# Performance work log

Hardware: AMD Instinct MI355X
Metric: run time of the kernel (lower is better)

Reference implementation:

```python
import jax, jax.numpy as jnp
import numpy as np

D_MODEL = 512
N_HEADS = 8
D_FF = 2048
B, L = 4, 2048
EPS = 1e-5


def _layernorm(x, g, b):
    mu = jnp.mean(x, axis=-1, keepdims=True)
    var = jnp.mean(jnp.square(x - mu), axis=-1, keepdims=True)
    return (x - mu) * jax.lax.rsqrt(var + EPS) * g + b


def setup_inputs() -> dict:
    key = jax.random.key(0)
    ks = jax.random.split(key, 8)
    s = 0.02
    return {
        'x': jax.random.normal(ks[0], (B, L, D_MODEL), jnp.float32),
        'Wq': jax.random.normal(ks[1], (D_MODEL, D_MODEL), jnp.float32) * s,
        'bq': jnp.zeros((D_MODEL,), jnp.float32),
        'Wk': jax.random.normal(ks[2], (D_MODEL, D_MODEL), jnp.float32) * s,
        'bk': jnp.zeros((D_MODEL,), jnp.float32),
        'Wv': jax.random.normal(ks[3], (D_MODEL, D_MODEL), jnp.float32) * s,
        'bv': jnp.zeros((D_MODEL,), jnp.float32),
        'Wo': jax.random.normal(ks[4], (D_MODEL, D_MODEL), jnp.float32) * s,
        'bo': jnp.zeros((D_MODEL,), jnp.float32),
        'W1': jax.random.normal(ks[5], (D_MODEL, D_FF), jnp.float32) * s,
        'b1': jnp.zeros((D_FF,), jnp.float32),
        'W2': jax.random.normal(ks[6], (D_FF, D_MODEL), jnp.float32) * s,
        'b2': jnp.zeros((D_MODEL,), jnp.float32),
        'g1': jnp.ones((D_MODEL,), jnp.float32),
        'be1': jnp.zeros((D_MODEL,), jnp.float32),
        'g2': jnp.ones((D_MODEL,), jnp.float32),
        'be2': jnp.zeros((D_MODEL,), jnp.float32),
    }


def reference(x, Wq, bq, Wk, bk, Wv, bv, Wo, bo, W1, b1, W2, b2, g1, be1, g2, be2):
    B_, L_, D = x.shape
    H = N_HEADS
    E = D // H
    q = (x @ Wq + bq).reshape(B_, L_, H, E)
    k = (x @ Wk + bk).reshape(B_, L_, H, E)
    v = (x @ Wv + bv).reshape(B_, L_, H, E)
    scale = 1.0 / jnp.sqrt(jnp.float32(E))
    # full [B,H,L,S] scores (mask_flag=False -> no causal mask)
    scores = jnp.einsum('blhe,bshe->bhls', q, k)
    A = jax.nn.softmax(scale * scores, axis=-1)
    V = jnp.einsum('bhls,bshd->blhd', A, v).reshape(B_, L_, D)
    attn_out = V @ Wo + bo
    x = _layernorm(x + attn_out, g1, be1)
    h = jax.nn.gelu(x @ W1 + b1, approximate=False)  # torch nn.GELU default = exact erf
    x = _layernorm(x + (h @ W2 + b2), g2, be2)
    return x
```

## Files before the change

kernel.cpp:

```cpp
#include <hip/hip_runtime.h>
#include <math.h>

#define DM 512
#define LSEQ 2048
#define BATCH 4
#define NH 8
#define EH 64
#define DFF 2048
#define MTOK (BATCH*LSEQ)
#define QKVW 1536
#define QSCL 0.18033688011112042f

using short8  = __attribute__((ext_vector_type(8))) short;
using floatx4 = __attribute__((ext_vector_type(4))) float;

__device__ __forceinline__ short f2b(float f) {
    unsigned u = __float_as_uint(f);
    return (short)((u + 0x7FFFu + ((u >> 16) & 1u)) >> 16);
}
__device__ __forceinline__ float b2f(short s) {
    return __uint_as_float(((unsigned)(unsigned short)s) << 16);
}
__device__ __forceinline__ unsigned pack2bf(float lo, float hi) {
    return __builtin_amdgcn_perm(__float_as_uint(hi) + 0x8000u,
                                 __float_as_uint(lo) + 0x8000u, 0x07060302u);
}
__device__ __forceinline__ float gelu_tanh(float v) {
    float v2 = v * v;
    float y  = v * fmaf(0.0356774081f, v2, 0.7978845608f);
    float e  = __builtin_amdgcn_exp2f(y * 2.885390082f);
    float r  = __builtin_amdgcn_rcpf(e + 1.0f);
    return v * (1.0f - r);
}
__device__ __forceinline__ void load_lds16(const short* g, short* l) {
    __builtin_amdgcn_global_load_lds(
        (const __attribute__((address_space(1))) void*)g,
        (__attribute__((address_space(3))) void*)l, 16, 0, 0);
}
#define MFMA_BF16(a, b, c) __builtin_amdgcn_mfma_f32_16x16x32_bf16(a, b, c, 0, 0, 0)

__global__ __launch_bounds__(256) void prep_kernel(
    const float* __restrict__ Wq, const float* __restrict__ Wk,
    const float* __restrict__ Wv, const float* __restrict__ Wo,
    const float* __restrict__ W1, const float* __restrict__ W2,
    const float* __restrict__ x,
    const float* __restrict__ bq, const float* __restrict__ bk,
    const float* __restrict__ bv,
    short* __restrict__ Wqkvt, short* __restrict__ Wot,
    short* __restrict__ W1t, short* __restrict__ W2t,
    short* __restrict__ xb, float* __restrict__ bqkv)
{
    __shared__ float t[64][65];
    const int bid = blockIdx.x;
    const int tid = threadIdx.x;

    if (bid >= 2880) {
        #pragma unroll
        for (int j = 0; j < 6; ++j) {
            const int i = j * 256 + tid;
            bqkv[i] = (i < 512) ? bq[i] : (i < 1024 ? bk[i - 512] : bv[i - 1024]);
        }
        return;
    }
    if (bid >= 832) {
        const long i = ((long)(bid - 832) * 256 + tid) * 8;
        float4 a = *(const float4*)(x + i);
        float4 b = *(const float4*)(x + i + 4);
        short tt[8] = { f2b(a.x), f2b(a.y), f2b(a.z), f2b(a.w),
                        f2b(b.x), f2b(b.y), f2b(b.z), f2b(b.w) };
        *(float4*)(xb + i) = *(float4*)tt;
        return;
    }
    const float* src; short* dst; int C, R, bx, by;
    if (bid < 256) {
        const int w = bid >> 6, sub = bid & 63;
        src = (w == 0) ? Wq : (w == 1) ? Wk : Wv;
        dst = Wqkvt + (long)w * 262144;
        R = 512; C = 512; bx = sub & 7; by = sub >> 3;
    } else if (bid < 320) {
        const int sub = bid - 256;
        src = Wo; dst = Wot; R = 512; C = 512; bx = sub & 7; by = sub >> 3;
    } else if (bid < 576) {
        const int sub = bid - 320;
        src = W1; dst = W1t; R = 512; C = 2048; bx = sub & 31; by = sub >> 5;
    } else {
        const int sub = bid - 576;
        src = W2; dst = W2t; R = 2048; C = 512; bx = sub & 7; by = sub >> 3;
    }
    const int r0 = by * 64, c0 = bx * 64;
    const int r = tid >> 2, cs = (tid & 3) * 16;
    const float* ip = src + (long)(r0 + r) * C + c0 + cs;
    #pragma unroll
    for (int i = 0; i < 4; ++i) {
        float4 v = *(const float4*)(ip + i * 4);
        t[r][cs + i*4 + 0] = v.x; t[r][cs + i*4 + 1] = v.y;
        t[r][cs + i*4 + 2] = v.z; t[r][cs + i*4 + 3] = v.w;
    }
    __syncthreads();
    short tmp[16];
    #pragma unroll
    for (int j = 0; j < 16; ++j) tmp[j] = f2b(t[cs + j][r]);
    short* op = dst + (long)(c0 + r) * R + r0 + cs;
    *(float4*)op       = *(float4*)&tmp[0];
    *(float4*)(op + 8) = *(float4*)&tmp[8];
}

template<int TN, int DO_GELU, int QKV>
__global__ __launch_bounds__(256, 4) void mfma_gemm(
    const short* __restrict__ A, const short* __restrict__ Bt,
    const float* __restrict__ bias, short* __restrict__ C,
    short* __restrict__ VtOut, int M, int N, int K, int lda, int ldc)
{
    constexpr int NJ = TN / 32;
    constexpr int NB = TN / 64;
    __shared__ short As[2][128][32];
    __shared__ short Bs[2][TN][32];

    const int tid  = threadIdx.x;
    const int wave = tid >> 6;
    const int lane = tid & 63;
    const int qd   = lane >> 4;
    const int sl   = lane & 15;
    const int m0 = blockIdx.y * 128;
    const int n0 = blockIdx.x * TN;
    const int wm = (wave & 1) * 64;
    const int wn = (wave >> 1) * (TN / 2);
    const int srow = lane >> 2;
    const int scol = (lane & 3) * 8;

    floatx4 acc[4][NJ];
    const floatx4 fz = {0.f, 0.f, 0.f, 0.f};
    #pragma unroll
    for (int i = 0; i < 4; ++i)
        #pragma unroll
        for (int j = 0; j < NJ; ++j) acc[i][j] = fz;

    const short* Abase = A  + (long)m0 * lda + scol;
    const short* Bbase = Bt + (long)n0 * K   + scol;

    #pragma unroll
    for (int it = 0; it < 2; ++it) {
        const int rg = wave * 2 + it;
        load_lds16(Abase + (long)(rg*16 + srow) * lda, &As[0][rg * 16][0]);
    }
    #pragma unroll
    for (int it = 0; it < NB; ++it) {
        const int rg = wave * NB + it;
        load_lds16(Bbase + (long)(rg*16 + srow) * K, &Bs[0][rg * 16][0]);
    }

    const int NIT = K / 32;
    for (int kit = 0; kit < NIT; ++kit) {
        const int cur = kit & 1;
        __syncthreads();
        if (kit + 1 < NIT) {
            const int nk = (kit + 1) * 32;
            #pragma unroll
            for (int it = 0; it < 2; ++it) {
                const int rg = wave * 2 + it;
                load_lds16(Abase + (long)(rg*16 + srow) * lda + nk, &As[1 - cur][rg * 16][0]);
            }
            #pragma unroll
            for (int it = 0; it < NB; ++it) {
                const int rg = wave * NB + it;
                load_lds16(Bbase + (long)(rg*16 + srow) * K + nk, &Bs[1 - cur][rg * 16][0]);
            }
        }
        short8 af[4], bf[NJ];
        #pragma unroll
        for (int t = 0; t < 4; ++t)
            af[t] = *(const short8*)&As[cur][wm + t*16 + sl][qd * 8];
        #pragma unroll
        for (int t = 0; t < NJ; ++t)
            bf[t] = *(const short8*)&Bs[cur][wn + t*16 + sl][qd * 8];
        #pragma unroll
        for (int i = 0; i < 4; ++i)
            #pragma unroll
            for (int j = 0; j < NJ; ++j)
                acc[i][j] = MFMA_BF16(af[i], bf[j], acc[i][j]);
    }

    #pragma unroll
    for (int j = 0; j < NJ; ++j) {
        const int col = n0 + wn + j*16 + sl;
        const float bvs = bias[col];
        #pragma unroll
        for (int i = 0; i < 4; ++i) {
            float v[4];
            #pragma unroll
            for (int r = 0; r < 4; ++r) {
                float tv = acc[i][j][r] + bvs;
                if (DO_GELU) tv = gelu_tanh(tv);
                v[r] = tv;
            }
            const int row0 = m0 + wm + i*16 + qd*4;
            if (QKV) {
                if (col < 1024) {
                    const float s = (col < 512) ? QSCL : 1.0f;
                    #pragma unroll
                    for (int r = 0; r < 4; ++r)
                        C[(long)(row0 + r) * 1024 + col] = f2b(v[r] * s);
                } else {
                    const int e = col - 1024;
                    const int b_ = row0 >> 11, l0 = row0 & 2047;
                    uint2 w;
                    w.x = pack2bf(v[0], v[1]);
                    w.y = pack2bf(v[2], v[3]);
                    *(uint2*)&VtOut[(((long)(b_*8 + (e >> 6))) * 64 + (e & 63)) * 2048 + l0] = w;
                }
            } else {
                #pragma unroll
                for (int r = 0; r < 4; ++r)
                    C[(long)(row0 + r) * ldc + col] = f2b(v[r]);
            }
        }
    }
}

__global__ __launch_bounds__(256, 2) void mfma_attn(
    const short* __restrict__ QK, const short* __restrict__ VtG,
    short* __restrict__ O)
{
    __shared__ short Ks[2][2][64][32];
    __shared__ short Vs[2][2][64][32];
    __shared__ short PT[4][32][72];

    const int tid  = threadIdx.x;
    const int wave = tid >> 6;
    const int lane = tid & 63;
    const int qd   = lane >> 4;
    const int sl   = lane & 15;
    const int srow = lane >> 2;
    const int scol = (lane & 3) * 8;

    const int bid = blockIdx.x;
    const int h  = bid & 7;
    const int b  = (bid >> 3) & 3;
    const int qt = bid >> 5;
    const int tok0 = b * LSEQ;
    const int q0 = qt * 128;

    const short* Kbase = QK + (long)tok0 * 1024 + 512 + h * EH
                         + (long)(wave*16 + srow) * 1024 + scol;
    const short* Vbase = VtG + ((long)(b * NH + h)) * EH * 2048
                         + (long)(wave*16 + srow) * 2048 + scol;

    {
        const int qr = lane >> 1;
        const int qc = (lane & 1) * 32;
        const short* qp = QK + (long)(tok0 + q0 + wave*32 + qr) * 1024 + h * EH + qc;
        short* dp = &PT[wave][qr][qc];
        *(float4*)dp        = *(const float4*)qp;
        *(float4*)(dp + 8)  = *(const float4*)(qp + 8);
        *(float4*)(dp + 16) = *(const float4*)(qp + 16);
        *(float4*)(dp + 24) = *(const float4*)(qp + 24);
    }
    short8 aq[2][2];
    #pragma unroll
    for (int q2 = 0; q2 < 2; ++q2)
        #pragma unroll
        for (int ks = 0; ks < 2; ++ks)
            aq[q2][ks] = *(const short8*)&PT[wave][q2*16 + sl][ks*32 + qd*8];

    float l_i[2] = {0.f, 0.f};
    floatx4 oacc[2][4];
    const floatx4 fz = {0.f, 0.f, 0.f, 0.f};
    #pragma unroll
    for (int q2 = 0; q2 < 2; ++q2)
        #pragma unroll
        for (int t = 0; t < 4; ++t) oacc[q2][t] = fz;

    #pragma unroll
    for (int p = 0; p < 2; ++p) {
        load_lds16(Kbase + p*32, &Ks[0][p][wave*16][0]);
        load_lds16(Vbase + p*32, &Vs[0][p][wave*16][0]);
    }

    for (int kt = 0; kt < 32; ++kt) {
        const int cur = kt & 1;
        __syncthreads();
        if (kt + 1 < 32) {
            #pragma unroll
            for (int p = 0; p < 2; ++p) {
                load_lds16(Kbase + (long)(kt+1)*64*1024 + p*32, &Ks[1 - cur][p][wave*16][0]);
                load_lds16(Vbase + (kt+1)*64 + p*32,            &Vs[1 - cur][p][wave*16][0]);
            }
        }

        floatx4 sT[2][4];
        #pragma unroll
        for (int q2 = 0; q2 < 2; ++q2)
            #pragma unroll
            for (int t = 0; t < 4; ++t) sT[q2][t] = fz;
        #pragma unroll
        for (int ks = 0; ks < 2; ++ks)
            #pragma unroll
            for (int t = 0; t < 4; ++t) {
                short8 ak = *(const short8*)&Ks[cur][ks][t*16 + sl][qd * 8];
                sT[0][t] = MFMA_BF16(ak, aq[0][ks], sT[0][t]);
                sT[1][t] = MFMA_BF16(ak, aq[1][ks], sT[1][t]);
            }

        #pragma unroll
        for (int q2 = 0; q2 < 2; ++q2)
            #pragma unroll
            for (int t = 0; t < 4; ++t) {
                const float p0 = __builtin_amdgcn_exp2f(sT[q2][t][0]);
                const float p1 = __builtin_amdgcn_exp2f(sT[q2][t][1]);
                const float p2 = __builtin_amdgcn_exp2f(sT[q2][t][2]);
                const float p3 = __builtin_amdgcn_exp2f(sT[q2][t][3]);
                l_i[q2] += (p0 + p1) + (p2 + p3);
                uint2 w;
                w.x = pack2bf(p0, p1);
                w.y = pack2bf(p2, p3);
                *(uint2*)&PT[wave][q2*16 + sl][t*16 + qd*4] = w;
            }

        #pragma unroll
        for (int ks = 0; ks < 2; ++ks) {
            short8 ap0 = *(const short8*)&PT[wave][sl][ks*32 + qd*8];
            short8 ap1 = *(const short8*)&PT[wave][16 + sl][ks*32 + qd*8];
            #pragma unroll
            for (int t = 0; t < 4; ++t) {
                short8 bv = *(const short8*)&Vs[cur][ks][t*16 + sl][qd * 8];
                oacc[0][t] = MFMA_BF16(ap0, bv, oacc[0][t]);
                oacc[1][t] = MFMA_BF16(ap1, bv, oacc[1][t]);
            }
        }
    }

    float linv[2][4];
    #pragma unroll
    for (int q2 = 0; q2 < 2; ++q2) {
        float l = l_i[q2];
        l += __shfl_xor(l, 16);
        l += __shfl_xor(l, 32);
        #pragma unroll
        for (int r = 0; r < 4; ++r)
            linv[q2][r] = 1.0f / __shfl(l, qd*4 + r, 64);
    }

    #pragma unroll
    for (int q2 = 0; q2 < 2; ++q2)
        #pragma unroll
        for (int t = 0; t < 4; ++t)
            #pragma unroll
            for (int r = 0; r < 4; ++r) {
                const int row = tok0 + q0 + wave*32 + q2*16 + qd*4 + r;
                const int col = h * EH + t*16 + sl;
                O[(long)row * DM + col] = f2b(oacc[q2][t][r] * linv[q2][r]);
            }
}

template<int X_BF16, int OUT_F32>
__global__ __launch_bounds__(256) void add_ln_kernel(
    const void* __restrict__ Xv, const short* __restrict__ R,
    const float* __restrict__ g, const float* __restrict__ beta,
    void* __restrict__ outv)
{
    const int row = blockIdx.x;
    const int tid = threadIdx.x;
    float x0, x1;
    if (X_BF16) {
        const short* xp = (const short*)Xv + (long)row * DM;
        x0 = b2f(xp[tid]); x1 = b2f(xp[tid + 256]);
    } else {
        const float* xp = (const float*)Xv + (long)row * DM;
        x0 = xp[tid]; x1 = xp[tid + 256];
    }
    const short* rp = R + (long)row * DM;
    const float v0 = x0 + b2f(rp[tid]);
    const float v1 = x1 + b2f(rp[tid + 256]);
    float s = v0 + v1, sq = v0*v0 + v1*v1;
    #pragma unroll
    for (int o = 32; o > 0; o >>= 1) {
        s  += __shfl_down(s, o);
        sq += __shfl_down(sq, o);
    }
    __shared__ float ss[4], ssq[4];
    const int wid = tid >> 6, lane = tid & 63;
    if (lane == 0) { ss[wid] = s; ssq[wid] = sq; }
    __syncthreads();
    const float S  = ss[0] + ss[1] + ss[2] + ss[3];
    const float SQ = ssq[0] + ssq[1] + ssq[2] + ssq[3];
    const float mean = S * (1.0f / DM);
    const float var  = SQ * (1.0f / DM) - mean * mean;
    const float rstd = rsqrtf(var + 1e-5f);
    const float o0 = (v0 - mean) * rstd * g[tid] + beta[tid];
    const float o1 = (v1 - mean) * rstd * g[tid + 256] + beta[tid + 256];
    if (OUT_F32) {
        float* op = (float*)outv + (long)row * DM;
        op[tid] = o0; op[tid + 256] = o1;
    } else {
        short* op = (short*)outv + (long)row * DM;
        op[tid] = f2b(o0); op[tid + 256] = f2b(o1);
    }
}

extern "C" void kernel_launch(void* const* d_in, const int* in_sizes, int n_in,
                              void* d_out, int out_size, void* d_ws, size_t ws_size,
                              hipStream_t stream)
{
    const float* x   = (const float*)d_in[0];
    const float* Wq  = (const float*)d_in[1];
    const float* bq  = (const float*)d_in[2];
    const float* Wk  = (const float*)d_in[3];
    const float* bk  = (const float*)d_in[4];
    const float* Wv  = (const float*)d_in[5];
    const float* bv  = (const float*)d_in[6];
    const float* Wo  = (const float*)d_in[7];
    const float* bo  = (const float*)d_in[8];
    const float* W1  = (const float*)d_in[9];
    const float* b1  = (const float*)d_in[10];
    const float* W2  = (const float*)d_in[11];
    const float* b2  = (const float*)d_in[12];
    const float* g1  = (const float*)d_in[13];
    const float* be1 = (const float*)d_in[14];
    const float* g2  = (const float*)d_in[15];
    const float* be2 = (const float*)d_in[16];
    float* out = (float*)d_out;

    short* ws    = (short*)d_ws;
    short* Wqkvt = ws;
    short* Wot   = Wqkvt + 786432;
    short* W1t   = Wot + 262144;
    short* W2t   = W1t + 1048576;
    float* bqkv  = (float*)(W2t + 1048576);
    short* xb    = (short*)(bqkv + 1536);
    short* qk    = xb + 4194304;
    short* VtG   = qk + 8388608;
    short* Ob    = VtG + 4194304;
    short* res   = Ob + 4194304;
    short* hbuf  = qk;

    const dim3 blk(256);

    prep_kernel<<<dim3(2881), blk, 0, stream>>>(
        Wq, Wk, Wv, Wo, W1, W2, x, bq, bk, bv,
        Wqkvt, Wot, W1t, W2t, xb, bqkv);

    mfma_gemm<128, 0, 1><<<dim3(12, 64), blk, 0, stream>>>(
        xb, Wqkvt, bqkv, qk, VtG, MTOK, QKVW, DM, DM, 0);

    mfma_attn<<<dim3(512), blk, 0, stream>>>(qk, VtG, Ob);

    mfma_gemm<64, 0, 0><<<dim3(8, 64), blk, 0, stream>>>(
        Ob, Wot, bo, res, nullptr, MTOK, DM, DM, DM, DM);

    add_ln_kernel<0, 0><<<dim3(MTOK), blk, 0, stream>>>(x, res, g1, be1, xb);

    mfma_gemm<128, 1, 0><<<dim3(16, 64), blk, 0, stream>>>(
        xb, W1t, b1, hbuf, nullptr, MTOK, DFF, DM, DM, DFF);

    mfma_gemm<64, 0, 0><<<dim3(8, 64), blk, 0, stream>>>(
        hbuf, W2t, b2, res, nullptr, MTOK, DM, DFF, DFF, DM);

    add_ln_kernel<1, 1><<<dim3(MTOK), blk, 0, stream>>>(xb, res, g2, be2, out);
}
```

Measured before the change: 276.7 us.

## Split attention over key halves with 8-wave blocks and a combine kernel

The attention kernel now uses 512-thread blocks covering 256 queries each, and splits the key sequence into two halves across blocks. The two partial unnormalized outputs and row sums are written to separate buffers, and a new combine kernel adds them, normalizes, and writes bf16 for the output projection. K loads are done by four waves and V loads by the other four, so each wave issues half as many loads. The aim is to halve K/V reloads per query and raise parallelism, at the cost of an extra kernel launch, extra memory traffic for partials, and a bf16 rounding step on the partial sums. It depends on the softmax being computed without a max subtraction, which the removed normalization suggests it is.

```diff
diff --git a/kernel.cpp b/kernel.cpp
--- a/kernel.cpp
+++ b/kernel.cpp
@@ -217,33 +217,37 @@
     }
 }
 
-__global__ __launch_bounds__(256, 2) void mfma_attn(
+__global__ __launch_bounds__(512, 2) void mfma_attn(
     const short* __restrict__ QK, const short* __restrict__ VtG,
-    short* __restrict__ O)
+    short* __restrict__ Op0, short* __restrict__ Op1, float* __restrict__ lbuf)
 {
     __shared__ short Ks[2][2][64][32];
     __shared__ short Vs[2][2][64][32];
-    __shared__ short PT[4][32][72];
+    __shared__ short PT[8][32][72];
 
     const int tid  = threadIdx.x;
     const int wave = tid >> 6;
     const int lane = tid & 63;
     const int qd   = lane >> 4;
     const int sl   = lane & 15;
+    const int kw   = wave & 3;
     const int srow = lane >> 2;
     const int scol = (lane & 3) * 8;
+    const bool is_v = wave >= 4;
 
     const int bid = blockIdx.x;
-    const int h  = bid & 7;
-    const int b  = (bid >> 3) & 3;
-    const int qt = bid >> 5;
+    const int h   = bid & 7;
+    const int b   = (bid >> 3) & 3;
+    const int qt  = (bid >> 5) & 7;
+    const int ksp = bid >> 8;
     const int tok0 = b * LSEQ;
-    const int q0 = qt * 128;
+    const int q0 = qt * 256;
+    const int kt0 = ksp * 16;
 
     const short* Kbase = QK + (long)tok0 * 1024 + 512 + h * EH
-                         + (long)(wave*16 + srow) * 1024 + scol;
+                         + (long)(kt0*64 + kw*16 + srow) * 1024 + scol;
     const short* Vbase = VtG + ((long)(b * NH + h)) * EH * 2048
-                         + (long)(wave*16 + srow) * 2048 + scol;
+                         + (long)(kw*16 + srow) * 2048 + kt0*64 + scol;
 
     {
         const int qr = lane >> 1;
@@ -270,20 +274,26 @@
         #pragma unroll
         for (int t = 0; t < 4; ++t) oacc[q2][t] = fz;
 
-    #pragma unroll
-    for (int p = 0; p < 2; ++p) {
-        load_lds16(Kbase + p*32, &Ks[0][p][wave*16][0]);
-        load_lds16(Vbase + p*32, &Vs[0][p][wave*16][0]);
-    }
-
-    for (int kt = 0; kt < 32; ++kt) {
+    if (!is_v) {
+        #pragma unroll
+        for (int p = 0; p < 2; ++p) load_lds16(Kbase + p*32, &Ks[0][p][kw*16][0]);
+    } else {
+        #pragma unroll
+        for (int p = 0; p < 2; ++p) load_lds16(Vbase + p*32, &Vs[0][p][kw*16][0]);
+    }
+
+    for (int kt = 0; kt < 16; ++kt) {
         const int cur = kt & 1;
         __syncthreads();
-        if (kt + 1 < 32) {
-            #pragma unroll
-            for (int p = 0; p < 2; ++p) {
-                load_lds16(Kbase + (long)(kt+1)*64*1024 + p*32, &Ks[1 - cur][p][wave*16][0]);
-                load_lds16(Vbase + (kt+1)*64 + p*32,            &Vs[1 - cur][p][wave*16][0]);
+        if (kt + 1 < 16) {
+            if (!is_v) {
+                #pragma unroll
+                for (int p = 0; p < 2; ++p)
+                    load_lds16(Kbase + (long)(kt+1)*64*1024 + p*32, &Ks[1 - cur][p][kw*16][0]);
+            } else {
+                #pragma unroll
+                for (int p = 0; p < 2; ++p)
+                    load_lds16(Vbase + (kt+1)*64 + p*32, &Vs[1 - cur][p][kw*16][0]);
             }
         }
 
@@ -329,15 +339,14 @@
         }
     }
 
-    float linv[2][4];
+    short* Op = ksp ? Op1 : Op0;
     #pragma unroll
     for (int q2 = 0; q2 < 2; ++q2) {
         float l = l_i[q2];
         l += __shfl_xor(l, 16);
         l += __shfl_xor(l, 32);
-        #pragma unroll
-        for (int r = 0; r < 4; ++r)
-            linv[q2][r] = 1.0f / __shfl(l, qd*4 + r, 64);
+        if (qd == 0)
+            lbuf[((long)ksp * MTOK + tok0 + q0 + wave*32 + q2*16 + sl) * 8 + h] = l;
     }
 
     #pragma unroll
@@ -348,8 +357,26 @@
             for (int r = 0; r < 4; ++r) {
                 const int row = tok0 + q0 + wave*32 + q2*16 + qd*4 + r;
                 const int col = h * EH + t*16 + sl;
-                O[(long)row * DM + col] = f2b(oacc[q2][t][r] * linv[q2][r]);
-            }
+                Op[(long)row * DM + col] = f2b(oacc[q2][t][r]);
+            }
+}
+
+__global__ __launch_bounds__(256) void attn_combine(
+    const short* __restrict__ Op0, const short* __restrict__ Op1,
+    const float* __restrict__ lbuf, short* __restrict__ Oc)
+{
+    const long idx = ((long)blockIdx.x * 256 + threadIdx.x) * 8;
+    const int row = (int)(idx >> 9);
+    const int h   = ((int)idx & 511) >> 6;
+    const float linv = 1.0f /
+        (lbuf[(long)row * 8 + h] + lbuf[((long)MTOK + row) * 8 + h]);
+    short a[8], c[8], o[8];
+    *(float4*)a = *(const float4*)(Op0 + idx);
+    *(float4*)c = *(const float4*)(Op1 + idx);
+    #pragma unroll
+    for (int i = 0; i < 8; ++i)
+        o[i] = f2b((b2f(a[i]) + b2f(c[i])) * linv);
+    *(float4*)(Oc + idx) = *(float4*)o;
 }
 
 template<int X_BF16, int OUT_F32>
@@ -431,6 +458,8 @@
     short* VtG   = qk + 8388608;
     short* Ob    = VtG + 4194304;
     short* res   = Ob + 4194304;
+    float* lbuf  = (float*)(res + 4194304);
+    short* Ocomb = qk;
     short* hbuf  = qk;
 
     const dim3 blk(256);
@@ -442,10 +471,12 @@
     mfma_gemm<128, 0, 1><<<dim3(12, 64), blk, 0, stream>>>(
         xb, Wqkvt, bqkv, qk, VtG, MTOK, QKVW, DM, DM, 0);
 
-    mfma_attn<<<dim3(512), blk, 0, stream>>>(qk, VtG, Ob);
+    mfma_attn<<<dim3(512), dim3(512), 0, stream>>>(qk, VtG, Ob, res, lbuf);
+
+    attn_combine<<<dim3(2048), blk, 0, stream>>>(Ob, res, lbuf, Ocomb);
 
     mfma_gemm<64, 0, 0><<<dim3(8, 64), blk, 0, stream>>>(
-        Ob, Wot, bo, res, nullptr, MTOK, DM, DM, DM, DM);
+        Ocomb, Wot, bo, res, nullptr, MTOK, DM, DM, DM, DM);
 
     add_ln_kernel<0, 0><<<dim3(MTOK), blk, 0, stream>>>(x, res, g1, be1, xb);
 
```

After: 270.6 us. 2.2% less time.
